# Kernel tuning notes

Hardware: AMD Instinct MI355X
Metric: run time of the kernel (lower is better)

The kernel has to match this reference:

```python
import jax, jax.numpy as jnp
import numpy as np

_LAYER_SHAPES = ((10, 8), (8, 8), (8, 1))


def setup_inputs() -> dict:
    key = jax.random.key(0)
    k1, k2, k3, k4 = jax.random.split(key, 4)
    B, D, H, W = 8, 8, 256, 256
    M = 256
    E = jax.random.normal(k1, (B, D, H, W), dtype=jnp.float32)
    theta = jax.random.normal(k2, (M, 169), dtype=jnp.float32)
    centers = jax.random.uniform(k3, (M, 2), dtype=jnp.float32)
    batch_index = jax.random.randint(k4, (M,), 0, B)
    return {"E": E, "theta": theta, "centers": centers, "batch_index": batch_index}


def reference(E, theta, centers, batch_index):
    B, D, H, W = E.shape
    M = theta.shape[0]
    dt = E.dtype
    # pixel-center grid in [0,1]: linspace(0.5/H, 1-0.5/H, H)
    ys = (jnp.arange(H, dtype=dt) + 0.5) / H
    xs = (jnp.arange(W, dtype=dt) + 0.5) / W
    grid_y, grid_x = jnp.meshgrid(ys, xs, indexing="ij")
    grid = jnp.stack([grid_x, grid_y], axis=0)  # (2, H, W), channel order (x, y)
    rel = grid[None] - centers.astype(dt)[:, :, None, None]  # (M, 2, H, W)

    e_per_match = E[batch_index]  # (M, D, H, W) gather
    x = jnp.concatenate([e_per_match, rel], axis=1)  # (M, D+2, H, W)

    # split flat theta into per-layer 1x1 conv weights/biases and apply
    offset = 0
    n_layers = len(_LAYER_SHAPES)
    for li, (c_in, c_out) in enumerate(_LAYER_SHAPES):
        w = theta[:, offset:offset + c_in * c_out].reshape(M, c_out, c_in)
        offset += c_in * c_out
        b = theta[:, offset:offset + c_out]
        offset += c_out
        # per-instance 1x1 conv == tiny batched matmul over channels
        x = jnp.einsum("moi,mihw->mohw", w, x) + b[:, :, None, None]
        if li < n_layers - 1:
            x = jax.nn.gelu(x, approximate=False)  # torch F.gelu default (erf)
    return x[:, 0]  # (M, H, W) mask logits
```

## Files before the change

kernel.cpp:

```cpp
#include <hip/hip_runtime.h>
#include <math.h>

#define HWPIX 65536
#define NMATCH 256
#define THETA_LEN 169

__device__ __forceinline__ float gelu_fast(float v) {
    float t = fmaf(v * v, 0.10294323f, 2.3022082f);
    float e = __builtin_amdgcn_exp2f(-v * t);
    float r = __builtin_amdgcn_rcpf(1.0f + e);
    return v * r;
}

__global__ __launch_bounds__(256) void dmh_kernel(
    const float* __restrict__ E,
    const float* __restrict__ theta,
    const float* __restrict__ centers,
    const int*   __restrict__ bidx,
    float* __restrict__ out)
{
    const int m    = blockIdx.x >> 6;
    const int tile = blockIdx.x & 63;
    const int p0   = tile * 1024 + threadIdx.x * 4;

    const float* __restrict__ th = theta + m * THETA_LEN;
    const float cx = centers[2 * m];
    const float cy = centers[2 * m + 1];
    const int   b  = bidx[m];
    const float* __restrict__ Eb = E + (size_t)b * (8 * HWPIX) + p0;

    const int h = p0 >> 8;
    const int w = p0 & 255;

    float x[10][4];
    #pragma unroll
    for (int c = 0; c < 8; ++c) {
        const float4 v = *(const float4*)(Eb + (size_t)c * HWPIX);
        x[c][0] = v.x; x[c][1] = v.y; x[c][2] = v.z; x[c][3] = v.w;
    }
    #pragma unroll
    for (int j = 0; j < 4; ++j) {
        x[8][j] = (w + j + 0.5f) * (1.0f / 256.0f) - cx;
        x[9][j] = (h + 0.5f) * (1.0f / 256.0f) - cy;
    }

    float y[8][4];
    #pragma unroll
    for (int o = 0; o < 8; ++o) {
        const float bias = th[80 + o];
        float a[4] = {bias, bias, bias, bias};
        #pragma unroll
        for (int i = 0; i < 10; ++i) {
            const float wv = th[o * 10 + i];
            #pragma unroll
            for (int j = 0; j < 4; ++j) a[j] = fmaf(wv, x[i][j], a[j]);
        }
        #pragma unroll
        for (int j = 0; j < 4; ++j) y[o][j] = gelu_fast(a[j]);
    }

    float z[8][4];
    #pragma unroll
    for (int o = 0; o < 8; ++o) {
        const float bias = th[152 + o];
        float a[4] = {bias, bias, bias, bias};
        #pragma unroll
        for (int i = 0; i < 8; ++i) {
            const float wv = th[88 + o * 8 + i];
            #pragma unroll
            for (int j = 0; j < 4; ++j) a[j] = fmaf(wv, y[i][j], a[j]);
        }
        #pragma unroll
        for (int j = 0; j < 4; ++j) z[o][j] = gelu_fast(a[j]);
    }

    const float b2 = th[168];
    float r[4] = {b2, b2, b2, b2};
    #pragma unroll
    for (int i = 0; i < 8; ++i) {
        const float wv = th[160 + i];
        #pragma unroll
        for (int j = 0; j < 4; ++j) r[j] = fmaf(wv, z[i][j], r[j]);
    }

    float4 o4;
    o4.x = r[0]; o4.y = r[1]; o4.z = r[2]; o4.w = r[3];
    *(float4*)(out + (size_t)m * HWPIX + p0) = o4;
}

extern "C" void kernel_launch(void* const* d_in, const int* in_sizes, int n_in,
                              void* d_out, int out_size, void* d_ws, size_t ws_size,
                              hipStream_t stream) {
    const float* E       = (const float*)d_in[0];
    const float* theta   = (const float*)d_in[1];
    const float* centers = (const float*)d_in[2];
    const int*   bidx    = (const int*)d_in[3];
    float* out = (float*)d_out;

    dim3 grid(NMATCH * 64);
    dim3 block(256);
    hipLaunchKernelGGL(dmh_kernel, grid, block, 0, stream, E, theta, centers, bidx, out);
}
```

Measured before the change: 170.5 us.

## Pack weights and activations to fp16 pairs and use fdot2 for channel mixing

```diff
diff --git a/kernel.cpp b/kernel.cpp
--- a/kernel.cpp
+++ b/kernel.cpp
@@ -4,6 +4,21 @@
 #define HWPIX 65536
 #define NMATCH 256
 #define THETA_LEN 169
+#define WSTRIDE 96
+
+typedef __fp16 half_t;
+typedef __fp16 half2_t __attribute__((ext_vector_type(2)));
+
+__device__ __forceinline__ unsigned int pack_rne(float a, float b) {
+    union { half2_t h; unsigned int u; } x;
+    x.h.x = (half_t)a;
+    x.h.y = (half_t)b;
+    return x.u;
+}
+
+__device__ __forceinline__ half2_t h2(unsigned int u) {
+    union { unsigned int u; half2_t h; } x; x.u = u; return x.h;
+}
 
 __device__ __forceinline__ float gelu_fast(float v) {
     float t = fmaf(v * v, 0.10294323f, 2.3022082f);
@@ -12,9 +27,36 @@
     return v * r;
 }
 
+__global__ __launch_bounds__(128) void prep_kernel(const float* __restrict__ theta,
+                                                   unsigned int* __restrict__ wpk) {
+    const int m = blockIdx.x;
+    const int t = threadIdx.x;
+    const float* __restrict__ th = theta + m * THETA_LEN;
+    unsigned int v = 0;
+    if (t < 40) {
+        const int o = t / 5, p = t % 5;
+        const int i0 = o * 10 + 2 * p;
+        v = pack_rne(th[i0], th[i0 + 1]);
+    } else if (t < 48) {
+        v = __float_as_uint(th[80 + (t - 40)]);
+    } else if (t < 80) {
+        const int q = t - 48, o = q / 4, p = q % 4;
+        const int i0 = 88 + o * 8 + 2 * p;
+        v = pack_rne(th[i0], th[i0 + 1]);
+    } else if (t < 88) {
+        v = __float_as_uint(th[152 + (t - 80)]);
+    } else if (t < 92) {
+        const int q = t - 88;
+        v = pack_rne(th[160 + 2 * q], th[161 + 2 * q]);
+    } else if (t == 92) {
+        v = __float_as_uint(th[168]);
+    }
+    if (t < 96) wpk[m * WSTRIDE + t] = v;
+}
+
 __global__ __launch_bounds__(256) void dmh_kernel(
     const float* __restrict__ E,
-    const float* __restrict__ theta,
+    const unsigned int* __restrict__ wpk,
     const float* __restrict__ centers,
     const int*   __restrict__ bidx,
     float* __restrict__ out)
@@ -23,7 +65,7 @@
     const int tile = blockIdx.x & 63;
     const int p0   = tile * 1024 + threadIdx.x * 4;
 
-    const float* __restrict__ th = theta + m * THETA_LEN;
+    const unsigned int* __restrict__ wm = wpk + m * WSTRIDE;
     const float cx = centers[2 * m];
     const float cy = centers[2 * m + 1];
     const int   b  = bidx[m];
@@ -32,55 +74,79 @@
     const int h = p0 >> 8;
     const int w = p0 & 255;
 
-    float x[10][4];
+    half2_t xp[5][4];
     #pragma unroll
-    for (int c = 0; c < 8; ++c) {
-        const float4 v = *(const float4*)(Eb + (size_t)c * HWPIX);
-        x[c][0] = v.x; x[c][1] = v.y; x[c][2] = v.z; x[c][3] = v.w;
+    for (int c = 0; c < 4; ++c) {
+        const float4 a0 = *(const float4*)(Eb + (size_t)(2 * c)     * HWPIX);
+        const float4 a1 = *(const float4*)(Eb + (size_t)(2 * c + 1) * HWPIX);
+        xp[c][0] = __builtin_amdgcn_cvt_pkrtz(a0.x, a1.x);
+        xp[c][1] = __builtin_amdgcn_cvt_pkrtz(a0.y, a1.y);
+        xp[c][2] = __builtin_amdgcn_cvt_pkrtz(a0.z, a1.z);
+        xp[c][3] = __builtin_amdgcn_cvt_pkrtz(a0.w, a1.w);
     }
+    const float ry = (h + 0.5f) * (1.0f / 256.0f) - cy;
     #pragma unroll
     for (int j = 0; j < 4; ++j) {
-        x[8][j] = (w + j + 0.5f) * (1.0f / 256.0f) - cx;
-        x[9][j] = (h + 0.5f) * (1.0f / 256.0f) - cy;
+        const float rx = (w + j + 0.5f) * (1.0f / 256.0f) - cx;
+        xp[4][j] = __builtin_amdgcn_cvt_pkrtz(rx, ry);
     }
 
-    float y[8][4];
+    half2_t yp[4][4];
     #pragma unroll
-    for (int o = 0; o < 8; ++o) {
-        const float bias = th[80 + o];
-        float a[4] = {bias, bias, bias, bias};
+    for (int oq = 0; oq < 4; ++oq) {
+        float g[2][4];
         #pragma unroll
-        for (int i = 0; i < 10; ++i) {
-            const float wv = th[o * 10 + i];
+        for (int s = 0; s < 2; ++s) {
+            const int o = 2 * oq + s;
+            const float bias = __uint_as_float(wm[40 + o]);
+            float a[4] = {bias, bias, bias, bias};
             #pragma unroll
-            for (int j = 0; j < 4; ++j) a[j] = fmaf(wv, x[i][j], a[j]);
+            for (int p = 0; p < 5; ++p) {
+                const half2_t wv = h2(wm[o * 5 + p]);
+                #pragma unroll
+                for (int j = 0; j < 4; ++j)
+                    a[j] = __builtin_amdgcn_fdot2(wv, xp[p][j], a[j], false);
+            }
+            #pragma unroll
+            for (int j = 0; j < 4; ++j) g[s][j] = gelu_fast(a[j]);
         }
         #pragma unroll
-        for (int j = 0; j < 4; ++j) y[o][j] = gelu_fast(a[j]);
+        for (int j = 0; j < 4; ++j)
+            yp[oq][j] = __builtin_amdgcn_cvt_pkrtz(g[0][j], g[1][j]);
     }
 
-    float z[8][4];
+    half2_t zp[4][4];
     #pragma unroll
-    for (int o = 0; o < 8; ++o) {
-        const float bias = th[152 + o];
-        float a[4] = {bias, bias, bias, bias};
+    for (int oq = 0; oq < 4; ++oq) {
+        float g[2][4];
         #pragma unroll
-        for (int i = 0; i < 8; ++i) {
-            const float wv = th[88 + o * 8 + i];
+        for (int s = 0; s < 2; ++s) {
+            const int o = 2 * oq + s;
+            const float bias = __uint_as_float(wm[80 + o]);
+            float a[4] = {bias, bias, bias, bias};
             #pragma unroll
-            for (int j = 0; j < 4; ++j) a[j] = fmaf(wv, y[i][j], a[j]);
+            for (int p = 0; p < 4; ++p) {
+                const half2_t wv = h2(wm[48 + o * 4 + p]);
+                #pragma unroll
+                for (int j = 0; j < 4; ++j)
+                    a[j] = __builtin_amdgcn_fdot2(wv, yp[p][j], a[j], false);
+            }
+            #pragma unroll
+            for (int j = 0; j < 4; ++j) g[s][j] = gelu_fast(a[j]);
         }
         #pragma unroll
-        for (int j = 0; j < 4; ++j) z[o][j] = gelu_fast(a[j]);
+        for (int j = 0; j < 4; ++j)
+            zp[oq][j] = __builtin_amdgcn_cvt_pkrtz(g[0][j], g[1][j]);
     }
 
-    const float b2 = th[168];
+    const float b2 = __uint_as_float(wm[92]);
     float r[4] = {b2, b2, b2, b2};
     #pragma unroll
-    for (int i = 0; i < 8; ++i) {
-        const float wv = th[160 + i];
+    for (int p = 0; p < 4; ++p) {
+        const half2_t wv = h2(wm[88 + p]);
         #pragma unroll
-        for (int j = 0; j < 4; ++j) r[j] = fmaf(wv, z[i][j], r[j]);
+        for (int j = 0; j < 4; ++j)
+            r[j] = __builtin_amdgcn_fdot2(wv, zp[p][j], r[j], false);
     }
 
     float4 o4;
@@ -96,8 +162,9 @@
     const float* centers = (const float*)d_in[2];
     const int*   bidx    = (const int*)d_in[3];
     float* out = (float*)d_out;
+    unsigned int* wpk = (unsigned int*)d_ws;
 
-    dim3 grid(NMATCH * 64);
-    dim3 block(256);
-    hipLaunchKernelGGL(dmh_kernel, grid, block, 0, stream, E, theta, centers, bidx, out);
+    hipLaunchKernelGGL(prep_kernel, dim3(NMATCH), dim3(128), 0, stream, theta, wpk);
+    hipLaunchKernelGGL(dmh_kernel, dim3(NMATCH * 64), dim3(256), 0, stream,
+                       E, wpk, centers, bidx, out);
 }
```

Result: slower. 187.6 us (+10.1%).
